# Kernel tuning notes

Measured on AMD Instinct MI355X. Metric: run time of the kernel, lower is better.

The kernel has to match this reference:

```python
import jax, jax.numpy as jnp
import numpy as np

N_EMBD = 1024
N_HEAD = 16
D_HEAD = N_EMBD // N_HEAD


def setup_inputs() -> dict:
    key = jax.random.key(0)
    ks = jax.random.split(key, 5)
    x = jax.random.normal(ks[0], (4, 2048, N_EMBD), dtype=jnp.float32)
    s = 1.0 / np.sqrt(N_EMBD)
    Wq = jax.random.normal(ks[1], (N_EMBD, N_EMBD), dtype=jnp.float32) * s
    Wk = jax.random.normal(ks[2], (N_EMBD, N_EMBD), dtype=jnp.float32) * s
    Wv = jax.random.normal(ks[3], (N_EMBD, N_EMBD), dtype=jnp.float32) * s
    Wo = jax.random.normal(ks[4], (N_EMBD, N_EMBD), dtype=jnp.float32) * s
    return {"x": x, "Wq": Wq, "Wk": Wk, "Wv": Wv, "Wo": Wo}


def reference(x, Wq, Wk, Wv, Wo):
    B, S, E = x.shape
    H, Dh = N_HEAD, D_HEAD
    scale = 1.0 / np.sqrt(Dh)  # LayerwiseSDPA(d_head) -> scale by 1/sqrt(d_head)

    def proj(W):
        # nn.Linear(no bias): y = x @ W.T ; reshape to [B,H,S,Dh]
        return (x @ W.T).reshape(B, S, H, Dh).transpose(0, 2, 1, 3)

    q, k, v = proj(Wq), proj(Wk), proj(Wv)
    scores = jnp.einsum('bhsd,bhtd->bhst', q, k) * scale  # [B,H,S,S]
    causal = jnp.tril(jnp.ones((S, S), dtype=bool))
    scores = jnp.where(causal, scores, jnp.finfo(scores.dtype).min)
    attn = jax.nn.softmax(scores, axis=-1)
    y = jnp.einsum('bhst,bhtd->bhsd', attn, v)  # [B,H,S,Dh]
    y = y.transpose(0, 2, 1, 3).reshape(B, S, E)
    return y @ Wo.T
```

## Files before the change

### kernel.cpp

```cpp
#include <hip/hip_runtime.h>

typedef __bf16 bf16;
typedef bf16  bf16x8 __attribute__((ext_vector_type(8)));
typedef bf16  bf16x4 __attribute__((ext_vector_type(4)));
typedef short s16x4  __attribute__((ext_vector_type(4)));
typedef float f32x4  __attribute__((ext_vector_type(4)));

#define AS1 __attribute__((address_space(1)))
#define AS3 __attribute__((address_space(3)))

#define SQLEN 2048
#define EMB   1024

__global__ __launch_bounds__(256) void cvt_f32_bf16(const float* __restrict__ in,
                                                    bf16* __restrict__ out, int n8) {
  int i = blockIdx.x * blockDim.x + threadIdx.x;
  if (i >= n8) return;
  const float4* p = (const float4*)in + (size_t)i * 2;
  float4 a = p[0], b = p[1];
  bf16x8 o;
  o[0] = (bf16)a.x; o[1] = (bf16)a.y; o[2] = (bf16)a.z; o[3] = (bf16)a.w;
  o[4] = (bf16)b.x; o[5] = (bf16)b.y; o[6] = (bf16)b.z; o[7] = (bf16)b.w;
  *((bf16x8*)out + i) = o;
}

__global__ __launch_bounds__(256) void cvt_w4(const float* __restrict__ w0, const float* __restrict__ w1,
                                              const float* __restrict__ w2, const float* __restrict__ w3,
                                              bf16* o0, bf16* o1, bf16* o2, bf16* o3, int n8) {
  const float* in; bf16* out;
  switch (blockIdx.y) {
    case 0: in = w0; out = o0; break;
    case 1: in = w1; out = o1; break;
    case 2: in = w2; out = o2; break;
    default: in = w3; out = o3; break;
  }
  int i = blockIdx.x * blockDim.x + threadIdx.x;
  if (i >= n8) return;
  const float4* p = (const float4*)in + (size_t)i * 2;
  float4 a = p[0], b = p[1];
  bf16x8 o;
  o[0] = (bf16)a.x; o[1] = (bf16)a.y; o[2] = (bf16)a.z; o[3] = (bf16)a.w;
  o[4] = (bf16)b.x; o[5] = (bf16)b.y; o[6] = (bf16)b.z; o[7] = (bf16)b.w;
  *((bf16x8*)out + i) = o;
}

template <int OUTF32>
__device__ __forceinline__
void gemm_body(const bf16* __restrict__ A, const bf16* __restrict__ B,
               float* __restrict__ Cf, bf16* __restrict__ Cb,
               int M, int N, int K, float scale, bf16* Asl, bf16* Bsl, int vtr) {
  const int tid  = threadIdx.x;
  const int lane = tid & 63, wave = tid >> 6;
  const int quad = lane >> 4, col = lane & 15;
  const int m0 = blockIdx.x * 128, n0 = blockIdx.y * 128;
  const int wr = wave >> 1, wc = wave & 1;

  f32x4 acc[4][4];
  const f32x4 fz = {0.f, 0.f, 0.f, 0.f};
#pragma unroll
  for (int i = 0; i < 4; ++i)
#pragma unroll
    for (int j = 0; j < 4; ++j) acc[i][j] = fz;

  const int srow = lane >> 2;
  const int sk   = lane & 3;

  auto stage = [&](int buf, int k0) {
#pragma unroll
    for (int r = 0; r < 2; ++r) {
      const int c      = wave * 2 + r;
      const int row    = c * 16 + srow;
      const int gchunk = sk ^ (row & 3);
      const bf16* ga = A + (size_t)(m0 + row) * K + k0 + gchunk * 8;
      const bf16* gb = B + (size_t)(n0 + row) * K + k0 + gchunk * 8;
      __builtin_amdgcn_global_load_lds((const AS1 void*)ga, (AS3 void*)(Asl + buf * 4096 + c * 512), 16, 0, 0);
      __builtin_amdgcn_global_load_lds((const AS1 void*)gb, (AS3 void*)(Bsl + buf * 4096 + c * 512), 16, 0, 0);
    }
  };

  const int nk = K >> 5;
  stage(0, 0);
  for (int it = 0; it < nk; ++it) {
    __syncthreads();
    if (it + 1 < nk) stage((it + 1) & 1, (it + 1) << 5);
    const bf16* As = Asl + (it & 1) * 4096;
    const bf16* Bs = Bsl + (it & 1) * 4096;

    bf16x8 af[4], bfr[4];
#pragma unroll
    for (int i = 0; i < 4; ++i) {
      const int r = wr * 64 + i * 16 + col;
      af[i] = *(const bf16x8*)&As[r * 32 + ((quad ^ (col & 3)) * 8)];
    }
#pragma unroll
    for (int j = 0; j < 4; ++j) {
      const int r = wc * 64 + j * 16 + col;
      bfr[j] = *(const bf16x8*)&Bs[r * 32 + ((quad ^ (col & 3)) * 8)];
    }
#pragma unroll
    for (int i = 0; i < 4; ++i)
#pragma unroll
      for (int j = 0; j < 4; ++j)
        acc[i][j] = __builtin_amdgcn_mfma_f32_16x16x32_bf16(af[i], bfr[j], acc[i][j], 0, 0, 0);
  }

#pragma unroll
  for (int i = 0; i < 4; ++i) {
#pragma unroll
    for (int j = 0; j < 4; ++j) {
      const int gm0 = m0 + wr * 64 + i * 16 + quad * 4;
      const int gn  = n0 + wc * 64 + j * 16 + col;
      if (OUTF32) {
#pragma unroll
        for (int r = 0; r < 4; ++r)
          Cf[(size_t)(gm0 + r) * N + gn] = acc[i][j][r] * scale;
      } else if (vtr) {
        bf16x4 ob;
#pragma unroll
        for (int r = 0; r < 4; ++r) ob[r] = (bf16)(acc[i][j][r] * scale);
        const int bb = gm0 >> 11;
        const int t_ = gm0 & 2047;
        *(bf16x4*)&Cb[((size_t)(bb * 1024 + gn)) * 2048 + t_] = ob;
      } else {
#pragma unroll
        for (int r = 0; r < 4; ++r)
          Cb[(size_t)(gm0 + r) * N + gn] = (bf16)(acc[i][j][r] * scale);
      }
    }
  }
}

__global__ __launch_bounds__(256, 2)
void gemm_qkv(const bf16* __restrict__ A, const bf16* __restrict__ Wq,
              const bf16* __restrict__ Wk, const bf16* __restrict__ Wv,
              bf16* Qo, bf16* Ko, bf16* Vto, float qscale) {
  __shared__ bf16 Asl[2 * 4096];
  __shared__ bf16 Bsl[2 * 4096];
  const bf16* B; bf16* C; float sc = 1.0f; int vtr = 0;
  if (blockIdx.z == 0)      { B = Wq; C = Qo; sc = qscale; }
  else if (blockIdx.z == 1) { B = Wk; C = Ko; }
  else                      { B = Wv; C = Vto; vtr = 1; }
  gemm_body<0>(A, B, nullptr, C, 8192, 1024, 1024, sc, Asl, Bsl, vtr);
}

__global__ __launch_bounds__(256, 2)
void gemm_o(const bf16* __restrict__ A, const bf16* __restrict__ W, float* __restrict__ C) {
  __shared__ bf16 Asl[2 * 4096];
  __shared__ bf16 Bsl[2 * 4096];
  gemm_body<1>(A, W, C, nullptr, 8192, 1024, 1024, 1.0f, Asl, Bsl, 0);
}

__global__ __launch_bounds__(512, 4)
void attn_flash(const bf16* __restrict__ Q, const bf16* __restrict__ K,
                const bf16* __restrict__ Vt, bf16* __restrict__ Y) {
  __shared__ bf16 smem[4 * 4096];
  bf16* Ksb0 = smem;
  bf16* Vsb0 = smem + 2 * 4096;

  const int tid  = threadIdx.x;
  const int lane = tid & 63, wave = tid >> 6;
  const int quad = lane >> 4, col = lane & 15;
  const int p  = blockIdx.x;
  const int h  = blockIdx.y;
  const int b  = blockIdx.z;
  const int hc = h * 64;
  const size_t rowBase = (size_t)b * SQLEN;

  const int srow8 = lane >> 3;
  const int sch   = lane & 7;
  const int gch   = sch ^ srow8;
  const int a7    = col & 7;

  auto stageKV = [&](int buf, int t0) {
    const int c  = wave;
    const int rr = c * 8 + srow8;
    const bf16* gk = K + (rowBase + t0 + rr) * EMB + hc + gch * 8;
    const bf16* gv = Vt + ((size_t)(b * EMB + hc + rr)) * SQLEN + t0 + gch * 8;
    __builtin_amdgcn_global_load_lds((const AS1 void*)gk, (AS3 void*)(Ksb0 + buf * 4096 + c * 512), 16, 0, 0);
    __builtin_amdgcn_global_load_lds((const AS1 void*)gv, (AS3 void*)(Vsb0 + buf * 4096 + c * 512), 16, 0, 0);
  };

#pragma unroll
  for (int halfIdx = 0; halfIdx < 2; ++halfIdx) {
    const int qt = halfIdx == 0 ? (15 - p) : p;
    const int q0 = qt * 128;

    stageKV(0, 0);

    bf16x8 qf0, qf1;
    {
      const int row = wave * 16 + col;
      const bf16* gq = Q + (rowBase + q0 + row) * EMB + hc + quad * 8;
      qf0 = *(const bf16x8*)gq;
      qf1 = *(const bf16x8*)(gq + 32);
    }
    __syncthreads();

    float m_i = -INFINITY, l_i = 0.f;
    f32x4 o[4];
    const f32x4 fz = {0.f, 0.f, 0.f, 0.f};
#pragma unroll
    for (int dd = 0; dd < 4; ++dd) o[dd] = fz;

    const int ntt = 2 * qt + 2;
    for (int tt = 0; tt < ntt; ++tt) {
      const int t0 = tt * 64;
      const int cur = tt & 1;
      if (tt + 1 < ntt) stageKV(cur ^ 1, t0 + 64);
      const bf16* Ks = Ksb0 + cur * 4096;
      const bf16* Vs = Vsb0 + cur * 4096;

      f32x4 s[4];
      __builtin_amdgcn_s_setprio(1);
#pragma unroll
      for (int sl = 0; sl < 4; ++sl) {
        const bf16x8 kf0 = *(const bf16x8*)&Ks[(sl * 16 + col) * 64 + ((quad ^ a7) * 8)];
        const bf16x8 kf1 = *(const bf16x8*)&Ks[(sl * 16 + col) * 64 + (((quad ^ 4) ^ a7) * 8)];
        f32x4 z = fz;
        z = __builtin_amdgcn_mfma_f32_16x16x32_bf16(kf0, qf0, z, 0, 0, 0);
        s[sl] = __builtin_amdgcn_mfma_f32_16x16x32_bf16(kf1, qf1, z, 0, 0, 0);
      }
      __builtin_amdgcn_s_setprio(0);

      if (tt >= 2 * qt) {
        const int qg = q0 + wave * 16 + col;
#pragma unroll
        for (int sl = 0; sl < 4; ++sl)
#pragma unroll
          for (int r = 0; r < 4; ++r)
            if (t0 + sl * 16 + quad * 4 + r > qg) s[sl][r] = -INFINITY;
      }

      bf16x4 pb[4];
      {
        float mx = s[0][0];
#pragma unroll
        for (int sl = 0; sl < 4; ++sl)
#pragma unroll
          for (int r = 0; r < 4; ++r) mx = fmaxf(mx, s[sl][r]);
        mx = fmaxf(mx, __shfl_xor(mx, 16));
        mx = fmaxf(mx, __shfl_xor(mx, 32));
        if (!__all(mx <= m_i + 8.f)) {
          const float mnew = fmaxf(m_i, mx);
          const float a = __builtin_amdgcn_exp2f(m_i - mnew);
          l_i *= a;
#pragma unroll
          for (int dd = 0; dd < 4; ++dd) o[dd] *= a;
          m_i = mnew;
        }
        float rs = 0.f;
#pragma unroll
        for (int sl = 0; sl < 4; ++sl)
#pragma unroll
          for (int r = 0; r < 4; ++r) {
            const float pv = __builtin_amdgcn_exp2f(s[sl][r] - m_i);
            rs += pv;
            pb[sl][r] = (bf16)pv;
          }
        rs += __shfl_xor(rs, 16);
        rs += __shfl_xor(rs, 32);
        l_i += rs;
      }

      __builtin_amdgcn_s_setprio(1);
#pragma unroll
      for (int sl = 0; sl < 4; ++sl) {
        const s16x4 pf = __builtin_bit_cast(s16x4, pb[sl]);
        const int cch  = 2 * sl + (quad >> 1);
        const int half = quad & 1;
#pragma unroll
        for (int dd = 0; dd < 4; ++dd) {
          const int row = dd * 16 + col;
          const bf16x4 vb = *(const bf16x4*)&Vs[row * 64 + ((cch ^ a7) * 8) + half * 4];
          const s16x4 vf = __builtin_bit_cast(s16x4, vb);
          o[dd] = __builtin_amdgcn_mfma_f32_16x16x16bf16_1k(vf, pf, o[dd], 0, 0, 0);
        }
      }
      __builtin_amdgcn_s_setprio(0);
      __syncthreads();
    }

    bf16* Ot = smem + wave * 1152;
    {
      const float rl = __builtin_amdgcn_rcpf(l_i);
#pragma unroll
      for (int dd = 0; dd < 4; ++dd) {
        bf16x4 ob;
#pragma unroll
        for (int r = 0; r < 4; ++r) ob[r] = (bf16)(o[dd][r] * rl);
        *(bf16x4*)&Ot[col * 72 + dd * 16 + quad * 4] = ob;
      }
#pragma unroll
      for (int i = 0; i < 2; ++i) {
        const int row = i * 8 + srow8;
        const bf16x8 v = *(const bf16x8*)&Ot[row * 72 + sch * 8];
        *(bf16x8*)&Y[(rowBase + q0 + wave * 16 + row) * EMB + hc + sch * 8] = v;
      }
    }
    if (halfIdx == 0) __syncthreads();
  }
}

extern "C" void kernel_launch(void* const* d_in, const int* in_sizes, int n_in,
                              void* d_out, int out_size, void* d_ws, size_t ws_size,
                              hipStream_t stream) {
  const float* x  = (const float*)d_in[0];
  const float* Wq = (const float*)d_in[1];
  const float* Wk = (const float*)d_in[2];
  const float* Wv = (const float*)d_in[3];
  const float* Wo = (const float*)d_in[4];
  float* out = (float*)d_out;

  const size_t ME = 8192ull * 1024ull;
  const size_t WE = 1024ull * 1024ull;
  bf16* ws  = (bf16*)d_ws;
  bf16* xb  = ws;
  bf16* wqb = xb + ME;
  bf16* wkb = wqb + WE;
  bf16* wvb = wkb + WE;
  bf16* wob = wvb + WE;
  bf16* Qb  = wob + WE;
  bf16* Kb  = Qb + ME;
  bf16* Vtb = Kb + ME;
  bf16* Yb  = Vtb + ME;

  cvt_f32_bf16<<<(int)(ME / 8 / 256), 256, 0, stream>>>(x, xb, (int)(ME / 8));
  cvt_w4<<<dim3((int)(WE / 8 / 256), 4), 256, 0, stream>>>(Wq, Wk, Wv, Wo, wqb, wkb, wvb, wob, (int)(WE / 8));

  const float qscale = 0.125f * 1.4426950408889634f;
  gemm_qkv<<<dim3(64, 8, 3), 256, 0, stream>>>(xb, wqb, wkb, wvb, Qb, Kb, Vtb, qscale);

  attn_flash<<<dim3(8, 16, 4), 512, 0, stream>>>(Qb, Kb, Vtb, Yb);

  gemm_o<<<dim3(64, 8), 256, 0, stream>>>(Yb, wob, out);
}
```

Baseline: 257.8 us.

## Load K tiles directly into registers with double-buffered prefetch, drop K LDS staging

K fragments are now read from global memory straight into registers, with the next tile prefetched during the current QK MFMAs through two ping-pong register sets. Only V is still staged through LDS, which halves shared memory use and could allow more resident blocks. The epilogue also writes Y directly from registers in 8-byte chunks instead of transposing through LDS, which removes a sync. The trade-offs are more vector registers, uncoalesced per-lane K loads repeated by every wave, and narrower global stores for Y.

```diff
diff --git a/kernel.cpp b/kernel.cpp
--- a/kernel.cpp
+++ b/kernel.cpp
@@ -153,9 +153,7 @@
 __global__ __launch_bounds__(512, 4)
 void attn_flash(const bf16* __restrict__ Q, const bf16* __restrict__ K,
                 const bf16* __restrict__ Vt, bf16* __restrict__ Y) {
-  __shared__ bf16 smem[4 * 4096];
-  bf16* Ksb0 = smem;
-  bf16* Vsb0 = smem + 2 * 4096;
+  __shared__ bf16 Vsb[2][64 * 64];
 
   const int tid  = threadIdx.x;
   const int lane = tid & 63, wave = tid >> 6;
@@ -171,21 +169,31 @@
   const int gch   = sch ^ srow8;
   const int a7    = col & 7;
 
-  auto stageKV = [&](int buf, int t0) {
-    const int c  = wave;
-    const int rr = c * 8 + srow8;
-    const bf16* gk = K + (rowBase + t0 + rr) * EMB + hc + gch * 8;
+  const bf16* Kbh = K + rowBase * EMB + hc;
+
+  auto stageV = [&](int buf, int t0) {
+    const int rr = wave * 8 + srow8;
     const bf16* gv = Vt + ((size_t)(b * EMB + hc + rr)) * SQLEN + t0 + gch * 8;
-    __builtin_amdgcn_global_load_lds((const AS1 void*)gk, (AS3 void*)(Ksb0 + buf * 4096 + c * 512), 16, 0, 0);
-    __builtin_amdgcn_global_load_lds((const AS1 void*)gv, (AS3 void*)(Vsb0 + buf * 4096 + c * 512), 16, 0, 0);
+    __builtin_amdgcn_global_load_lds((const AS1 void*)gv, (AS3 void*)(&Vsb[buf][wave * 512]), 16, 0, 0);
   };
 
-#pragma unroll
+  auto loadK = [&](bf16x8 (&k0)[4], bf16x8 (&k1)[4], int t0) {
+#pragma unroll
+    for (int sl = 0; sl < 4; ++sl) {
+      const bf16* gk = Kbh + (size_t)(t0 + sl * 16 + col) * EMB + quad * 8;
+      k0[sl] = *(const bf16x8*)gk;
+      k1[sl] = *(const bf16x8*)(gk + 32);
+    }
+  };
+
   for (int halfIdx = 0; halfIdx < 2; ++halfIdx) {
     const int qt = halfIdx == 0 ? (15 - p) : p;
     const int q0 = qt * 128;
-
-    stageKV(0, 0);
+    const int ntt = 2 * qt + 2;
+
+    bf16x8 kA0[4], kA1[4], kB0[4], kB1[4];
+    loadK(kA0, kA1, 0);
+    stageV(0, 0);
 
     bf16x8 qf0, qf1;
     {
@@ -202,25 +210,24 @@
 #pragma unroll
     for (int dd = 0; dd < 4; ++dd) o[dd] = fz;
 
-    const int ntt = 2 * qt + 2;
-    for (int tt = 0; tt < ntt; ++tt) {
+    auto iterBody = [&](const bf16x8 (&c0)[4], const bf16x8 (&c1)[4],
+                        bf16x8 (&n0)[4], bf16x8 (&n1)[4], int tt) {
       const int t0 = tt * 64;
       const int cur = tt & 1;
-      if (tt + 1 < ntt) stageKV(cur ^ 1, t0 + 64);
-      const bf16* Ks = Ksb0 + cur * 4096;
-      const bf16* Vs = Vsb0 + cur * 4096;
+      if (tt + 1 < ntt) stageV(cur ^ 1, t0 + 64);
+      const bf16* Vs = &Vsb[cur][0];
 
       f32x4 s[4];
       __builtin_amdgcn_s_setprio(1);
 #pragma unroll
       for (int sl = 0; sl < 4; ++sl) {
-        const bf16x8 kf0 = *(const bf16x8*)&Ks[(sl * 16 + col) * 64 + ((quad ^ a7) * 8)];
-        const bf16x8 kf1 = *(const bf16x8*)&Ks[(sl * 16 + col) * 64 + (((quad ^ 4) ^ a7) * 8)];
         f32x4 z = fz;
-        z = __builtin_amdgcn_mfma_f32_16x16x32_bf16(kf0, qf0, z, 0, 0, 0);
-        s[sl] = __builtin_amdgcn_mfma_f32_16x16x32_bf16(kf1, qf1, z, 0, 0, 0);
+        z = __builtin_amdgcn_mfma_f32_16x16x32_bf16(c0[sl], qf0, z, 0, 0, 0);
+        s[sl] = __builtin_amdgcn_mfma_f32_16x16x32_bf16(c1[sl], qf1, z, 0, 0, 0);
       }
       __builtin_amdgcn_s_setprio(0);
+
+      if (tt + 1 < ntt) loadK(n0, n1, t0 + 64);
 
       if (tt >= 2 * qt) {
         const int qg = q0 + wave * 16 + col;
@@ -278,26 +285,24 @@
       }
       __builtin_amdgcn_s_setprio(0);
       __syncthreads();
-    }
-
-    bf16* Ot = smem + wave * 1152;
+    };
+
+    for (int tt = 0; tt < ntt; tt += 2) {
+      iterBody(kA0, kA1, kB0, kB1, tt);
+      iterBody(kB0, kB1, kA0, kA1, tt + 1);
+    }
+
     {
       const float rl = __builtin_amdgcn_rcpf(l_i);
+      const size_t yrow = (rowBase + q0 + wave * 16 + col) * EMB + hc;
 #pragma unroll
       for (int dd = 0; dd < 4; ++dd) {
         bf16x4 ob;
 #pragma unroll
         for (int r = 0; r < 4; ++r) ob[r] = (bf16)(o[dd][r] * rl);
-        *(bf16x4*)&Ot[col * 72 + dd * 16 + quad * 4] = ob;
-      }
-#pragma unroll
-      for (int i = 0; i < 2; ++i) {
-        const int row = i * 8 + srow8;
-        const bf16x8 v = *(const bf16x8*)&Ot[row * 72 + sch * 8];
-        *(bf16x8*)&Y[(rowBase + q0 + wave * 16 + row) * EMB + hc + sch * 8] = v;
-      }
-    }
-    if (halfIdx == 0) __syncthreads();
+        *(bf16x4*)&Y[yrow + dd * 16 + quad * 4] = ob;
+      }
+    }
   }
 }
 
```

Result: slower. 339.5 us (+31.7%).

## Widen attention KV tile to 128, compute row sums via MFMA, remap blocks

Applied to the files above, without the earlier changes.

The flash attention loop now processes 128 keys per iteration instead of 64, doubling the shared-memory K/V buffers and halving the number of barriers and softmax rescale checks. The row-sum reduction is replaced by an extra MFMA against a ones vector, which removes the cross-lane shuffles. The output is written straight to global memory instead of being staged through LDS, and blocks are linearised with a swizzled mapping of batch, head and query pair. The costs are higher LDS use per block, which may lower occupancy, more masked wasted work on the diagonal tile, and narrower global stores.

```diff
diff --git a/kernel.cpp b/kernel.cpp
--- a/kernel.cpp
+++ b/kernel.cpp
@@ -153,37 +153,47 @@
 __global__ __launch_bounds__(512, 4)
 void attn_flash(const bf16* __restrict__ Q, const bf16* __restrict__ K,
                 const bf16* __restrict__ Vt, bf16* __restrict__ Y) {
-  __shared__ bf16 smem[4 * 4096];
-  bf16* Ksb0 = smem;
-  bf16* Vsb0 = smem + 2 * 4096;
+  __shared__ bf16 Ksb0[2 * 8192];
+  __shared__ bf16 Vsb0[2 * 8192];
 
   const int tid  = threadIdx.x;
   const int lane = tid & 63, wave = tid >> 6;
   const int quad = lane >> 4, col = lane & 15;
-  const int p  = blockIdx.x;
-  const int h  = blockIdx.y;
-  const int b  = blockIdx.z;
+
+  const int B_ = blockIdx.x;
+  const int bh = (B_ & 7) * 8 + (B_ >> 6);
+  const int p  = (B_ >> 3) & 7;
+  const int h  = bh & 15;
+  const int b  = bh >> 4;
   const int hc = h * 64;
   const size_t rowBase = (size_t)b * SQLEN;
 
   const int srow8 = lane >> 3;
   const int sch   = lane & 7;
-  const int gch   = sch ^ srow8;
   const int a7    = col & 7;
 
   auto stageKV = [&](int buf, int t0) {
-    const int c  = wave;
-    const int rr = c * 8 + srow8;
-    const bf16* gk = K + (rowBase + t0 + rr) * EMB + hc + gch * 8;
-    const bf16* gv = Vt + ((size_t)(b * EMB + hc + rr)) * SQLEN + t0 + gch * 8;
-    __builtin_amdgcn_global_load_lds((const AS1 void*)gk, (AS3 void*)(Ksb0 + buf * 4096 + c * 512), 16, 0, 0);
-    __builtin_amdgcn_global_load_lds((const AS1 void*)gv, (AS3 void*)(Vsb0 + buf * 4096 + c * 512), 16, 0, 0);
+#pragma unroll
+    for (int i = 0; i < 2; ++i) {
+      const int krow = wave * 16 + i * 8 + srow8;
+      const int kch  = sch ^ srow8;
+      const bf16* gk = K + (rowBase + t0 + krow) * EMB + hc + kch * 8;
+      __builtin_amdgcn_global_load_lds((const AS1 void*)gk,
+          (AS3 void*)(Ksb0 + buf * 8192 + wave * 1024 + i * 512), 16, 0, 0);
+      const int vrow = wave * 8 + i * 4 + (lane >> 4);
+      const int vch  = (lane & 15) ^ (vrow & 7);
+      const bf16* gv = Vt + ((size_t)(b * EMB + hc + vrow)) * SQLEN + t0 + vch * 8;
+      __builtin_amdgcn_global_load_lds((const AS1 void*)gv,
+          (AS3 void*)(Vsb0 + buf * 8192 + wave * 1024 + i * 512), 16, 0, 0);
+    }
   };
 
-#pragma unroll
+  const s16x4 ones = {(short)0x3F80, (short)0x3F80, (short)0x3F80, (short)0x3F80};
+
   for (int halfIdx = 0; halfIdx < 2; ++halfIdx) {
     const int qt = halfIdx == 0 ? (15 - p) : p;
     const int q0 = qt * 128;
+    const int ntt = qt + 1;
 
     stageKV(0, 0);
 
@@ -196,24 +206,24 @@
     }
     __syncthreads();
 
-    float m_i = -INFINITY, l_i = 0.f;
-    f32x4 o[4];
+    float m_i = -INFINITY;
+    f32x4 o[4], ol;
     const f32x4 fz = {0.f, 0.f, 0.f, 0.f};
 #pragma unroll
     for (int dd = 0; dd < 4; ++dd) o[dd] = fz;
-
-    const int ntt = 2 * qt + 2;
+    ol = fz;
+
     for (int tt = 0; tt < ntt; ++tt) {
-      const int t0 = tt * 64;
+      const int t0 = tt * 128;
       const int cur = tt & 1;
-      if (tt + 1 < ntt) stageKV(cur ^ 1, t0 + 64);
-      const bf16* Ks = Ksb0 + cur * 4096;
-      const bf16* Vs = Vsb0 + cur * 4096;
-
-      f32x4 s[4];
+      if (tt + 1 < ntt) stageKV(cur ^ 1, t0 + 128);
+      const bf16* Ks = Ksb0 + cur * 8192;
+      const bf16* Vs = Vsb0 + cur * 8192;
+
+      f32x4 s[8];
       __builtin_amdgcn_s_setprio(1);
 #pragma unroll
-      for (int sl = 0; sl < 4; ++sl) {
+      for (int sl = 0; sl < 8; ++sl) {
         const bf16x8 kf0 = *(const bf16x8*)&Ks[(sl * 16 + col) * 64 + ((quad ^ a7) * 8)];
         const bf16x8 kf1 = *(const bf16x8*)&Ks[(sl * 16 + col) * 64 + (((quad ^ 4) ^ a7) * 8)];
         f32x4 z = fz;
@@ -222,20 +232,20 @@
       }
       __builtin_amdgcn_s_setprio(0);
 
-      if (tt >= 2 * qt) {
+      if (tt == qt) {
         const int qg = q0 + wave * 16 + col;
 #pragma unroll
-        for (int sl = 0; sl < 4; ++sl)
+        for (int sl = 0; sl < 8; ++sl)
 #pragma unroll
           for (int r = 0; r < 4; ++r)
             if (t0 + sl * 16 + quad * 4 + r > qg) s[sl][r] = -INFINITY;
       }
 
-      bf16x4 pb[4];
+      bf16x4 pb[8];
       {
         float mx = s[0][0];
 #pragma unroll
-        for (int sl = 0; sl < 4; ++sl)
+        for (int sl = 0; sl < 8; ++sl)
 #pragma unroll
           for (int r = 0; r < 4; ++r) mx = fmaxf(mx, s[sl][r]);
         mx = fmaxf(mx, __shfl_xor(mx, 16));
@@ -243,35 +253,29 @@
         if (!__all(mx <= m_i + 8.f)) {
           const float mnew = fmaxf(m_i, mx);
           const float a = __builtin_amdgcn_exp2f(m_i - mnew);
-          l_i *= a;
 #pragma unroll
           for (int dd = 0; dd < 4; ++dd) o[dd] *= a;
+          ol *= a;
           m_i = mnew;
         }
-        float rs = 0.f;
-#pragma unroll
-        for (int sl = 0; sl < 4; ++sl)
-#pragma unroll
-          for (int r = 0; r < 4; ++r) {
-            const float pv = __builtin_amdgcn_exp2f(s[sl][r] - m_i);
-            rs += pv;
-            pb[sl][r] = (bf16)pv;
-          }
-        rs += __shfl_xor(rs, 16);
-        rs += __shfl_xor(rs, 32);
-        l_i += rs;
+#pragma unroll
+        for (int sl = 0; sl < 8; ++sl)
+#pragma unroll
+          for (int r = 0; r < 4; ++r)
+            pb[sl][r] = (bf16)__builtin_amdgcn_exp2f(s[sl][r] - m_i);
       }
 
       __builtin_amdgcn_s_setprio(1);
 #pragma unroll
-      for (int sl = 0; sl < 4; ++sl) {
+      for (int sl = 0; sl < 8; ++sl) {
         const s16x4 pf = __builtin_bit_cast(s16x4, pb[sl]);
+        ol = __builtin_amdgcn_mfma_f32_16x16x16bf16_1k(ones, pf, ol, 0, 0, 0);
         const int cch  = 2 * sl + (quad >> 1);
         const int half = quad & 1;
 #pragma unroll
         for (int dd = 0; dd < 4; ++dd) {
           const int row = dd * 16 + col;
-          const bf16x4 vb = *(const bf16x4*)&Vs[row * 64 + ((cch ^ a7) * 8) + half * 4];
+          const bf16x4 vb = *(const bf16x4*)&Vs[row * 128 + ((cch ^ a7) * 8) + half * 4];
           const s16x4 vf = __builtin_bit_cast(s16x4, vb);
           o[dd] = __builtin_amdgcn_mfma_f32_16x16x16bf16_1k(vf, pf, o[dd], 0, 0, 0);
         }
@@ -280,24 +284,17 @@
       __syncthreads();
     }
 
-    bf16* Ot = smem + wave * 1152;
     {
-      const float rl = __builtin_amdgcn_rcpf(l_i);
+      const float rl = __builtin_amdgcn_rcpf(ol[0]);
+      const size_t yrow = (rowBase + q0 + wave * 16 + col) * EMB + hc;
 #pragma unroll
       for (int dd = 0; dd < 4; ++dd) {
         bf16x4 ob;
 #pragma unroll
         for (int r = 0; r < 4; ++r) ob[r] = (bf16)(o[dd][r] * rl);
-        *(bf16x4*)&Ot[col * 72 + dd * 16 + quad * 4] = ob;
-      }
-#pragma unroll
-      for (int i = 0; i < 2; ++i) {
-        const int row = i * 8 + srow8;
-        const bf16x8 v = *(const bf16x8*)&Ot[row * 72 + sch * 8];
-        *(bf16x8*)&Y[(rowBase + q0 + wave * 16 + row) * EMB + hc + sch * 8] = v;
-      }
-    }
-    if (halfIdx == 0) __syncthreads();
+        *(bf16x4*)&Y[yrow + dd * 16 + quad * 4] = ob;
+      }
+    }
   }
 }
 
@@ -330,7 +327,7 @@
   const float qscale = 0.125f * 1.4426950408889634f;
   gemm_qkv<<<dim3(64, 8, 3), 256, 0, stream>>>(xb, wqb, wkb, wvb, Qb, Kb, Vtb, qscale);
 
-  attn_flash<<<dim3(8, 16, 4), 512, 0, stream>>>(Qb, Kb, Vtb, Yb);
+  attn_flash<<<512, 512, 0, stream>>>(Qb, Kb, Vtb, Yb);
 
   gemm_o<<<dim3(64, 8), 256, 0, stream>>>(Yb, wob, out);
 }
```

After: 251.4 us. 1.03x faster.
